# Kernel tuning notes

Measured on AMD Instinct MI355X. Metric: run time of the kernel, lower is better.

Reference implementation:

```python
import jax, jax.numpy as jnp
import numpy as np

# physical and transform constants (from BVPModel fields / zpinn globals)
_C0 = 343.0   # speed of sound
_RHO0 = 1.21  # air density (unused in r_net)
FC, F0 = 500.0, 100.0
XC, YC, ZC = 0.7, 0.5, 0.6
AC, A0 = 2.0, 0.1
BC, B0 = 1.5, -0.05

N = 131072
H = 256


def setup_inputs() -> dict:
    key = jax.random.key(0)
    ks = jax.random.split(key, 10)
    inp = {
        "x": jax.random.uniform(ks[0], (N,), jnp.float32),
        "y": jax.random.uniform(ks[1], (N,), jnp.float32),
        "z": jax.random.uniform(ks[2], (N,), jnp.float32),
        "f": jax.random.uniform(ks[3], (N,), jnp.float32),
        # MLP params, scaled by 1/sqrt(fan_in) (glorot-ish)
        "W1": jax.random.normal(ks[4], (H, 4), jnp.float32) / np.sqrt(4.0),
        "b1": jnp.zeros((H,), jnp.float32),
        "W2": jax.random.normal(ks[5], (H, H), jnp.float32) / np.sqrt(H),
        "b2": jnp.zeros((H,), jnp.float32),
        "W3": jax.random.normal(ks[6], (H, H), jnp.float32) / np.sqrt(H),
        "b3": jnp.zeros((H,), jnp.float32),
        "W4": jax.random.normal(ks[7], (2, H), jnp.float32) / np.sqrt(H),
        "b4": jnp.zeros((2,), jnp.float32),
    }
    return inp


def _psi(params, x, y, z, f):
    """Scalar-coordinate MLP: psi(x,y,z,f) -> (2,) [real, imag]."""
    h = jnp.stack([x, y, z, f])
    for (W, b) in params[:-1]:
        h = jnp.tanh(W @ h + b)
    W, b = params[-1]
    return W @ h + b


def reference(x, y, z, f, W1, b1, W2, b2, W3, b3, W4, b4):
    params = ((W1, b1), (W2, b2), (W3, b3), (W4, b4))

    def r_net(xi, yi, zi, fi):
        k = 2.0 * jnp.pi * (fi * FC + F0) / _C0
        pr, pi = _psi(params, xi, yi, zi, fi)

        fr = lambda a, b_, c, d: _psi(params, a, b_, c, d)[0]
        fim = lambda a, b_, c, d: _psi(params, a, b_, c, d)[1]
        d2 = lambda fn, i: jax.grad(jax.grad(fn, i), i)

        p_xxr = d2(fr, 0)(xi, yi, zi, fi)
        p_yyr = d2(fr, 1)(xi, yi, zi, fi)
        p_zzr = d2(fr, 2)(xi, yi, zi, fi)
        res_re = AC * ((YC * ZC) ** 2 * p_xxr
                       + (XC * ZC) ** 2 * p_yyr
                       + (XC * YC) ** 2 * p_zzr) \
            + (XC * YC * ZC * k) ** 2 * (pr * AC + A0)

        p_xxi = d2(fim, 0)(xi, yi, zi, fi)
        p_yyi = d2(fim, 1)(xi, yi, zi, fi)
        p_zzi = d2(fim, 2)(xi, yi, zi, fi)
        res_im = BC * ((YC * ZC) ** 2 * p_xxi
                       + (XC * ZC) ** 2 * p_yyi
                       + (XC * YC) ** 2 * p_zzi) \
            + (XC * YC * ZC * k) ** 2 * (pi * BC + B0)
        return res_re, res_im

    rr, ri = jax.vmap(r_net)(x, y, z, f)
    return jnp.stack([rr, ri])  # (2, N)
```

## Files before the change

### kernel.cpp

```cpp
#include <hip/hip_runtime.h>
#include <math.h>


typedef __attribute__((ext_vector_type(8))) short short8;
typedef __attribute__((ext_vector_type(4))) float floatx4;
typedef unsigned short ushort_t;
typedef unsigned int uint_t;

#define PBLK 16
#define NS 5

#define CXX 0.09f
#define CYY 0.1764f
#define CZZ 0.1225f

__device__ __forceinline__ ushort_t f2bf(float f) {
    uint_t u = __float_as_uint(f);
    return (ushort_t)((u + 0x7FFFu + ((u >> 16) & 1u)) >> 16);
}
__device__ __forceinline__ uint_t pack2bf(float f0, float f1) {
    uint_t u0 = __float_as_uint(f0) + 0x8000u;
    uint_t u1 = __float_as_uint(f1) + 0x8000u;
    return __builtin_amdgcn_perm(u1, u0, 0x07060302u);
}
__device__ __forceinline__ float fast_tanh(float u) {
    float e = __expf(2.f * u);
    return (e - 1.f) * __builtin_amdgcn_rcpf(e + 1.f);
}

__global__ void prep_split(const float* __restrict__ W2, const float* __restrict__ W3,
                           short8* __restrict__ ws) {
    int t16 = blockIdx.x * blockDim.x + threadIdx.x;
    int lane = t16 & 63;
    int kc = (t16 >> 6) & 7;
    int tt = (t16 >> 9) & 15;
    int l = t16 >> 13;
    const float* W = l ? W3 : W2;
    int row = tt * 16 + (lane & 15);
    int qa = lane >> 4;
    const float* src = W + row * 256 + kc * 32 + (l ? 4 * qa : 8 * qa);
    float4 va = *(const float4*)src;
    float4 vb = *(const float4*)(src + (l ? 16 : 4));
    float v[8] = {va.x, va.y, va.z, va.w, vb.x, vb.y, vb.z, vb.w};
    short8 hi8;
    #pragma unroll
    for (int j = 0; j < 8; ++j) hi8[j] = (short)f2bf(v[j]);
    ws[l * 8192 + tt * 512 + kc * 64 + lane] = hi8;
}

__global__ __launch_bounds__(512, 6)
void bvp_main(const float* __restrict__ gx, const float* __restrict__ gy,
              const float* __restrict__ gz, const float* __restrict__ gf,
              const float* __restrict__ W1, const float* __restrict__ b1,
              const float* __restrict__ b2, const float* __restrict__ b3,
              const float* __restrict__ W4, const float* __restrict__ b4,
              const short8* __restrict__ wsA, float* __restrict__ out, int N) {
    __shared__ short8 Bsh[NS * 8 * 64];
    __shared__ float red[8][16][4];

    const int tid = threadIdx.x;
    const int w = tid >> 6, lane = tid & 63;
    const int n15 = lane & 15, qc = lane >> 4;
    const int pbase = blockIdx.x * PBLK;
    const short8* __restrict__ wsA3 = wsA + 8192;

    floatx4 acc[2][NS];

    {
        const int pp = tid & 15, u8 = tid >> 4;
        const int kt = u8 >> 2, qb = u8 & 3;
        const int pidx = min(pbase + pp, N - 1);
        const float xi = gx[pidx], yi = gy[pidx], zi = gz[pidx], fi = gf[pidx];
        uint_t* const Bw = (uint_t*)Bsh;
        const int base4 = ((kt * 64) + qb * 16 + pp) * 4;
        #pragma unroll
        for (int rp = 0; rp < 4; ++rp) {
            const int i0 = u8 * 8 + 2 * rp;
            float4 wa = *(const float4*)(W1 + 4 * i0);
            float4 wb = *(const float4*)(W1 + 4 * i0 + 4);
            float u0 = fmaf(wa.x, xi, fmaf(wa.y, yi, fmaf(wa.z, zi, fmaf(wa.w, fi, b1[i0]))));
            float u1 = fmaf(wb.x, xi, fmaf(wb.y, yi, fmaf(wb.z, zi, fmaf(wb.w, fi, b1[i0 + 1]))));
            float t0 = fast_tanh(u0), s0 = 1.f - t0 * t0, c0 = -2.f * t0 * s0;
            float t1 = fast_tanh(u1), s1 = 1.f - t1 * t1, c1 = -2.f * t1 * s1;
            float wq0 = fmaf(CXX * wa.x, wa.x, fmaf(CYY * wa.y, wa.y, CZZ * wa.z * wa.z));
            float wq1 = fmaf(CXX * wb.x, wb.x, fmaf(CYY * wb.y, wb.y, CZZ * wb.z * wb.z));
            Bw[base4 + 0 * 2048 + rp] = pack2bf(t0, t1);
            Bw[base4 + 1 * 2048 + rp] = pack2bf(s0 * wa.x, s1 * wb.x);
            Bw[base4 + 2 * 2048 + rp] = pack2bf(s0 * wa.y, s1 * wb.y);
            Bw[base4 + 3 * 2048 + rp] = pack2bf(s0 * wa.z, s1 * wb.z);
            Bw[base4 + 4 * 2048 + rp] = pack2bf(c0 * wq0, c1 * wq1);
        }
    }
    __syncthreads();

    auto run_gemm = [&](const short8* __restrict__ A) {
        #pragma unroll
        for (int rt = 0; rt < 2; ++rt)
            #pragma unroll
            for (int ct = 0; ct < NS; ++ct) acc[rt][ct] = (floatx4){0.f, 0.f, 0.f, 0.f};
        #pragma unroll
        for (int kc = 0; kc < 8; ++kc) {
            short8 av[2];
            #pragma unroll
            for (int rt = 0; rt < 2; ++rt)
                av[rt] = A[(2 * w + rt) * 512 + kc * 64 + lane];
            #pragma unroll
            for (int ct = 0; ct < NS; ++ct) {
                const short8 b = Bsh[(ct * 8 + kc) * 64 + lane];
                #pragma unroll
                for (int rt = 0; rt < 2; ++rt)
                    acc[rt][ct] = __builtin_amdgcn_mfma_f32_16x16x32_bf16(av[rt], b, acc[rt][ct], 0, 0, 0);
            }
        }
    };

    run_gemm(wsA);
    __syncthreads();

    #pragma unroll
    for (int rt = 0; rt < 2; ++rt) {
        const float4 bb = *(const float4*)(b2 + w * 32 + rt * 16 + qc * 4);
        const float bbv[4] = {bb.x, bb.y, bb.z, bb.w};
        #pragma unroll
        for (int r = 0; r < 4; ++r) {
            float t = fast_tanh(acc[rt][0][r] + bbv[r]);
            float s = 1.f - t * t, c = -2.f * t * s;
            float ux = acc[rt][1][r], uy = acc[rt][2][r], uz = acc[rt][3][r];
            float wq = fmaf(CXX * ux, ux, fmaf(CYY * uy, uy, CZZ * uz * uz));
            acc[rt][0][r] = t;
            acc[rt][1][r] = s * ux; acc[rt][2][r] = s * uy; acc[rt][3][r] = s * uz;
            acc[rt][4][r] = fmaf(s, acc[rt][4][r], c * wq);
        }
    }
    #pragma unroll
    for (int s = 0; s < NS; ++s) {
        union { short8 s8; uint_t u4[4]; } v;
        v.u4[0] = pack2bf(acc[0][s][0], acc[0][s][1]);
        v.u4[1] = pack2bf(acc[0][s][2], acc[0][s][3]);
        v.u4[2] = pack2bf(acc[1][s][0], acc[1][s][1]);
        v.u4[3] = pack2bf(acc[1][s][2], acc[1][s][3]);
        Bsh[(s * 8 + w) * 64 + lane] = v.s8;
    }
    __syncthreads();

    run_gemm(wsA3);

    float pt[4] = {0.f, 0.f, 0.f, 0.f};
    #pragma unroll
    for (int rt = 0; rt < 2; ++rt) {
        const int rb = w * 32 + rt * 16 + qc * 4;
        const float4 bb = *(const float4*)(b3 + rb);
        const float4 w0 = *(const float4*)(W4 + rb);
        const float4 w1 = *(const float4*)(W4 + 256 + rb);
        const float bbv[4] = {bb.x, bb.y, bb.z, bb.w};
        const float w0v[4] = {w0.x, w0.y, w0.z, w0.w};
        const float w1v[4] = {w1.x, w1.y, w1.z, w1.w};
        #pragma unroll
        for (int r = 0; r < 4; ++r) {
            float t = fast_tanh(acc[rt][0][r] + bbv[r]);
            float s = 1.f - t * t, c = -2.f * t * s;
            float ux = acc[rt][1][r], uy = acc[rt][2][r], uz = acc[rt][3][r];
            float wq = fmaf(CXX * ux, ux, fmaf(CYY * uy, uy, CZZ * uz * uz));
            float hL = fmaf(s, acc[rt][4][r], c * wq);
            pt[0] = fmaf(w0v[r], t, pt[0]);
            pt[1] = fmaf(w0v[r], hL, pt[1]);
            pt[2] = fmaf(w1v[r], t, pt[2]);
            pt[3] = fmaf(w1v[r], hL, pt[3]);
        }
    }
    #pragma unroll
    for (int k = 0; k < 4; ++k) {
        pt[k] += __shfl_xor(pt[k], 16, 64);
        pt[k] += __shfl_xor(pt[k], 32, 64);
    }
    if (qc == 0)
        *(float4*)&red[w][n15][0] = make_float4(pt[0], pt[1], pt[2], pt[3]);
    __syncthreads();

    if (tid < 16 && (pbase + tid) < N) {
        const int n = pbase + tid;
        float s4[4] = {0.f, 0.f, 0.f, 0.f};
        #pragma unroll
        for (int ww = 0; ww < 8; ++ww)
            #pragma unroll
            for (int k = 0; k < 4; ++k) s4[k] += red[ww][tid][k];
        const float fi = gf[n];
        const float PI = 3.14159265358979323846f;
        const float kw = 2.f * PI * (fi * 500.f + 100.f) / 343.f;
        const float vol = 0.7f * 0.5f * 0.6f;
        const float kk = vol * vol * kw * kw;
        const float pr = s4[0] + b4[0];
        const float pim = s4[2] + b4[1];
        out[n]     = 2.0f * s4[1] + kk * (pr * 2.0f + 0.1f);
        out[N + n] = 1.5f * s4[3] + kk * (pim * 1.5f - 0.05f);
    }
}

extern "C" void kernel_launch(void* const* d_in, const int* in_sizes, int n_in,
                              void* d_out, int out_size, void* d_ws, size_t ws_size,
                              hipStream_t stream) {
    const float* x = (const float*)d_in[0];
    const float* y = (const float*)d_in[1];
    const float* z = (const float*)d_in[2];
    const float* f = (const float*)d_in[3];
    const float* W1 = (const float*)d_in[4];
    const float* b1 = (const float*)d_in[5];
    const float* W2 = (const float*)d_in[6];
    const float* b2 = (const float*)d_in[7];
    const float* W3 = (const float*)d_in[8];
    const float* b3 = (const float*)d_in[9];
    const float* W4 = (const float*)d_in[10];
    const float* b4 = (const float*)d_in[11];
    float* out = (float*)d_out;
    const int N = in_sizes[0];
    const int grid = (N + PBLK - 1) / PBLK;

    prep_split<<<64, 256, 0, stream>>>(W2, W3, (short8*)d_ws);
    bvp_main<<<grid, 512, 0, stream>>>(x, y, z, f, W1, b1, b2, b3, W4, b4,
                                       (const short8*)d_ws, out, N);
}
```

Measured before the change: 259.8 us.

## Double points per block and widen per-wave row tiles for weight reuse

Each block now processes 32 points instead of 16. The 8 waves split into two point-halves of four row-groups, and each wave computes 4 row tiles (64 rows) instead of 2. This halves the A-operand (weight) fetches per point and improves register-level reuse of the B fragments from LDS. The cost is double the accumulator registers per thread (launch bounds lowered from 6 to 4) and a larger shared-memory buffer. The reduction scratch now aliases that buffer, which needs an extra barrier.

```diff
diff --git a/kernel.cpp b/kernel.cpp
--- a/kernel.cpp
+++ b/kernel.cpp
@@ -7,7 +7,7 @@
 typedef unsigned short ushort_t;
 typedef unsigned int uint_t;
 
-#define PBLK 16
+#define PBLK 32
 #define NS 5
 
 #define CXX 0.09f
@@ -48,67 +48,72 @@
     ws[l * 8192 + tt * 512 + kc * 64 + lane] = hi8;
 }
 
-__global__ __launch_bounds__(512, 6)
+__global__ __launch_bounds__(512, 4)
 void bvp_main(const float* __restrict__ gx, const float* __restrict__ gy,
               const float* __restrict__ gz, const float* __restrict__ gf,
               const float* __restrict__ W1, const float* __restrict__ b1,
               const float* __restrict__ b2, const float* __restrict__ b3,
               const float* __restrict__ W4, const float* __restrict__ b4,
               const short8* __restrict__ wsA, float* __restrict__ out, int N) {
-    __shared__ short8 Bsh[NS * 8 * 64];
-    __shared__ float red[8][16][4];
+    __shared__ short8 Bsh[2][NS * 8 * 64];
+    float (*red)[4][16][4] = (float (*)[4][16][4])Bsh;
 
     const int tid = threadIdx.x;
     const int w = tid >> 6, lane = tid & 63;
+    const int rg = w & 3, ph = w >> 2;
     const int n15 = lane & 15, qc = lane >> 4;
     const int pbase = blockIdx.x * PBLK;
     const short8* __restrict__ wsA3 = wsA + 8192;
 
-    floatx4 acc[2][NS];
+    floatx4 acc[4][NS];
 
     {
-        const int pp = tid & 15, u8 = tid >> 4;
-        const int kt = u8 >> 2, qb = u8 & 3;
-        const int pidx = min(pbase + pp, N - 1);
+        const int pp = tid & 15, php = (tid >> 4) & 1;
+        const int pidx = min(pbase + php * 16 + pp, N - 1);
         const float xi = gx[pidx], yi = gy[pidx], zi = gz[pidx], fi = gf[pidx];
         uint_t* const Bw = (uint_t*)Bsh;
-        const int base4 = ((kt * 64) + qb * 16 + pp) * 4;
-        #pragma unroll
-        for (int rp = 0; rp < 4; ++rp) {
-            const int i0 = u8 * 8 + 2 * rp;
-            float4 wa = *(const float4*)(W1 + 4 * i0);
-            float4 wb = *(const float4*)(W1 + 4 * i0 + 4);
-            float u0 = fmaf(wa.x, xi, fmaf(wa.y, yi, fmaf(wa.z, zi, fmaf(wa.w, fi, b1[i0]))));
-            float u1 = fmaf(wb.x, xi, fmaf(wb.y, yi, fmaf(wb.z, zi, fmaf(wb.w, fi, b1[i0 + 1]))));
-            float t0 = fast_tanh(u0), s0 = 1.f - t0 * t0, c0 = -2.f * t0 * s0;
-            float t1 = fast_tanh(u1), s1 = 1.f - t1 * t1, c1 = -2.f * t1 * s1;
-            float wq0 = fmaf(CXX * wa.x, wa.x, fmaf(CYY * wa.y, wa.y, CZZ * wa.z * wa.z));
-            float wq1 = fmaf(CXX * wb.x, wb.x, fmaf(CYY * wb.y, wb.y, CZZ * wb.z * wb.z));
-            Bw[base4 + 0 * 2048 + rp] = pack2bf(t0, t1);
-            Bw[base4 + 1 * 2048 + rp] = pack2bf(s0 * wa.x, s1 * wb.x);
-            Bw[base4 + 2 * 2048 + rp] = pack2bf(s0 * wa.y, s1 * wb.y);
-            Bw[base4 + 3 * 2048 + rp] = pack2bf(s0 * wa.z, s1 * wb.z);
-            Bw[base4 + 4 * 2048 + rp] = pack2bf(c0 * wq0, c1 * wq1);
+        #pragma unroll
+        for (int g = 0; g < 2; ++g) {
+            const int u8 = (tid >> 5) + 16 * g;
+            const int kt = u8 >> 2, qb = u8 & 3;
+            const int base4 = php * 10240 + (kt * 64 + qb * 16 + pp) * 4;
+            #pragma unroll
+            for (int rp = 0; rp < 4; ++rp) {
+                const int i0 = u8 * 8 + 2 * rp;
+                float4 wa = *(const float4*)(W1 + 4 * i0);
+                float4 wb = *(const float4*)(W1 + 4 * i0 + 4);
+                float u0 = fmaf(wa.x, xi, fmaf(wa.y, yi, fmaf(wa.z, zi, fmaf(wa.w, fi, b1[i0]))));
+                float u1 = fmaf(wb.x, xi, fmaf(wb.y, yi, fmaf(wb.z, zi, fmaf(wb.w, fi, b1[i0 + 1]))));
+                float t0 = fast_tanh(u0), s0 = 1.f - t0 * t0, c0 = -2.f * t0 * s0;
+                float t1 = fast_tanh(u1), s1 = 1.f - t1 * t1, c1 = -2.f * t1 * s1;
+                float wq0 = fmaf(CXX * wa.x, wa.x, fmaf(CYY * wa.y, wa.y, CZZ * wa.z * wa.z));
+                float wq1 = fmaf(CXX * wb.x, wb.x, fmaf(CYY * wb.y, wb.y, CZZ * wb.z * wb.z));
+                Bw[base4 + 0 * 2048 + rp] = pack2bf(t0, t1);
+                Bw[base4 + 1 * 2048 + rp] = pack2bf(s0 * wa.x, s1 * wb.x);
+                Bw[base4 + 2 * 2048 + rp] = pack2bf(s0 * wa.y, s1 * wb.y);
+                Bw[base4 + 3 * 2048 + rp] = pack2bf(s0 * wa.z, s1 * wb.z);
+                Bw[base4 + 4 * 2048 + rp] = pack2bf(c0 * wq0, c1 * wq1);
+            }
         }
     }
     __syncthreads();
 
     auto run_gemm = [&](const short8* __restrict__ A) {
         #pragma unroll
-        for (int rt = 0; rt < 2; ++rt)
+        for (int rt = 0; rt < 4; ++rt)
             #pragma unroll
             for (int ct = 0; ct < NS; ++ct) acc[rt][ct] = (floatx4){0.f, 0.f, 0.f, 0.f};
         #pragma unroll
         for (int kc = 0; kc < 8; ++kc) {
-            short8 av[2];
-            #pragma unroll
-            for (int rt = 0; rt < 2; ++rt)
-                av[rt] = A[(2 * w + rt) * 512 + kc * 64 + lane];
+            short8 av[4];
+            #pragma unroll
+            for (int rt = 0; rt < 4; ++rt)
+                av[rt] = A[(rg * 4 + rt) * 512 + kc * 64 + lane];
             #pragma unroll
             for (int ct = 0; ct < NS; ++ct) {
-                const short8 b = Bsh[(ct * 8 + kc) * 64 + lane];
+                const short8 b = Bsh[ph][(ct * 8 + kc) * 64 + lane];
                 #pragma unroll
-                for (int rt = 0; rt < 2; ++rt)
+                for (int rt = 0; rt < 4; ++rt)
                     acc[rt][ct] = __builtin_amdgcn_mfma_f32_16x16x32_bf16(av[rt], b, acc[rt][ct], 0, 0, 0);
             }
         }
@@ -118,8 +123,8 @@
     __syncthreads();
 
     #pragma unroll
-    for (int rt = 0; rt < 2; ++rt) {
-        const float4 bb = *(const float4*)(b2 + w * 32 + rt * 16 + qc * 4);
+    for (int rt = 0; rt < 4; ++rt) {
+        const float4 bb = *(const float4*)(b2 + rg * 64 + rt * 16 + qc * 4);
         const float bbv[4] = {bb.x, bb.y, bb.z, bb.w};
         #pragma unroll
         for (int r = 0; r < 4; ++r) {
@@ -133,22 +138,24 @@
         }
     }
     #pragma unroll
-    for (int s = 0; s < NS; ++s) {
-        union { short8 s8; uint_t u4[4]; } v;
-        v.u4[0] = pack2bf(acc[0][s][0], acc[0][s][1]);
-        v.u4[1] = pack2bf(acc[0][s][2], acc[0][s][3]);
-        v.u4[2] = pack2bf(acc[1][s][0], acc[1][s][1]);
-        v.u4[3] = pack2bf(acc[1][s][2], acc[1][s][3]);
-        Bsh[(s * 8 + w) * 64 + lane] = v.s8;
-    }
+    for (int s = 0; s < NS; ++s)
+        #pragma unroll
+        for (int kt2 = 0; kt2 < 2; ++kt2) {
+            union { short8 s8; uint_t u4[4]; } v;
+            v.u4[0] = pack2bf(acc[2 * kt2][s][0], acc[2 * kt2][s][1]);
+            v.u4[1] = pack2bf(acc[2 * kt2][s][2], acc[2 * kt2][s][3]);
+            v.u4[2] = pack2bf(acc[2 * kt2 + 1][s][0], acc[2 * kt2 + 1][s][1]);
+            v.u4[3] = pack2bf(acc[2 * kt2 + 1][s][2], acc[2 * kt2 + 1][s][3]);
+            Bsh[ph][(s * 8 + 2 * rg + kt2) * 64 + lane] = v.s8;
+        }
     __syncthreads();
 
     run_gemm(wsA3);
 
     float pt[4] = {0.f, 0.f, 0.f, 0.f};
     #pragma unroll
-    for (int rt = 0; rt < 2; ++rt) {
-        const int rb = w * 32 + rt * 16 + qc * 4;
+    for (int rt = 0; rt < 4; ++rt) {
+        const int rb = rg * 64 + rt * 16 + qc * 4;
         const float4 bb = *(const float4*)(b3 + rb);
         const float4 w0 = *(const float4*)(W4 + rb);
         const float4 w1 = *(const float4*)(W4 + 256 + rb);
@@ -173,17 +180,19 @@
         pt[k] += __shfl_xor(pt[k], 16, 64);
         pt[k] += __shfl_xor(pt[k], 32, 64);
     }
+    __syncthreads();
     if (qc == 0)
-        *(float4*)&red[w][n15][0] = make_float4(pt[0], pt[1], pt[2], pt[3]);
-    __syncthreads();
-
-    if (tid < 16 && (pbase + tid) < N) {
+        *(float4*)&red[ph][rg][n15][0] = make_float4(pt[0], pt[1], pt[2], pt[3]);
+    __syncthreads();
+
+    if (tid < 32 && (pbase + tid) < N) {
         const int n = pbase + tid;
+        const int ph2 = tid >> 4, i15 = tid & 15;
         float s4[4] = {0.f, 0.f, 0.f, 0.f};
         #pragma unroll
-        for (int ww = 0; ww < 8; ++ww)
-            #pragma unroll
-            for (int k = 0; k < 4; ++k) s4[k] += red[ww][tid][k];
+        for (int rr = 0; rr < 4; ++rr)
+            #pragma unroll
+            for (int k = 0; k < 4; ++k) s4[k] += red[ph2][rr][i15][k];
         const float fi = gf[n];
         const float PI = 3.14159265358979323846f;
         const float kw = 2.f * PI * (fi * 500.f + 100.f) / 343.f;
```

Measured after the change: 270.9 us. +4.3%, slower.
